# Optimization experiments

Hardware: AMD Instinct MI355X
Metric: run time of the kernel (lower is better)

Reference implementation:

```python
import jax, jax.numpy as jnp
import numpy as np

B, NS, NC = 4096, 1024, 256
GUMBEL_HARD = True


def _linear(x, W, b):
    # torch nn.Linear: y = x @ W.T + b, W is [out, in]
    return x @ W.T + b


def _gumbel_softmax(logits, gnoise, tau, hard):
    y = jax.nn.softmax((logits + gnoise) / tau, axis=-1)
    if hard:
        y_hard = jax.nn.one_hot(jnp.argmax(y, axis=-1), y.shape[-1], dtype=y.dtype)
        y = y_hard + y - jax.lax.stop_gradient(y)  # straight-through
    return y


def setup_inputs() -> dict:
    key = jax.random.key(0)
    ks = jax.random.split(key, 32)
    inp = {
        "ct": jax.random.normal(ks[0], (B, NC), jnp.float32),
        "b1": jax.random.uniform(ks[1], (B, 2), jnp.float32),
        "b2": jax.random.uniform(ks[2], (B, 2), jnp.float32),
        "b3": jax.random.uniform(ks[3], (B, 2), jnp.float32),
        "rnn1": jax.random.normal(ks[4], (B, NS), jnp.float32),
        "rnn2": jax.random.normal(ks[5], (B, NS), jnp.float32),
        "rnn3": jax.random.normal(ks[6], (B, NS), jnp.float32),
        "rnn4": jax.random.normal(ks[7], (B, NS), jnp.float32),
        "gn1": jax.random.gumbel(ks[8], (B, 2), jnp.float32),
        "gn2": jax.random.gumbel(ks[9], (B, 2), jnp.float32),
        "gn3": jax.random.gumbel(ks[10], (B, 2), jnp.float32),
        "theta": 1,
    }
    def lin(k, out_d, in_d):
        return (0.02 * jax.random.normal(k, (out_d, in_d), jnp.float32),
                jnp.zeros((out_d,), jnp.float32))
    shapes = {
        "e_ct": (NS, NC), "rnn1_b0": (NS, 2 * NS), "rnn1_b1": (NS, 2 * NS),
        "b1_rnn1": (2, NS), "rnn2_b0": (NS, 2 * NS), "rnn2_b1": (NS, 2 * NS),
        "b2_rnn2": (2, NS), "rnn3_b0": (NS, 2 * NS), "rnn3_b1": (NS, 2 * NS),
        "b3_rnn3": (2, NS), "rnn4": (NS, 2 * NS), "hg_rnns": (NS, 4 * NS),
        "g_hg": (4, NS), "hctpi_rnns": (NS, 4 * NS), "ctpi_hctpi": (NC, NS),
    }
    for i, (name, (o, ii)) in enumerate(shapes.items()):
        W, bb = lin(ks[11 + i], o, ii)
        inp["W_" + name] = W
        inp["b_" + name] = bb
    return inp


def reference(ct, b1, b2, b3, rnn1, rnn2, rnn3, rnn4, gn1, gn2, gn3, theta,
              W_e_ct, b_e_ct, W_rnn1_b0, b_rnn1_b0, W_rnn1_b1, b_rnn1_b1,
              W_b1_rnn1, b_b1_rnn1, W_rnn2_b0, b_rnn2_b0, W_rnn2_b1, b_rnn2_b1,
              W_b2_rnn2, b_b2_rnn2, W_rnn3_b0, b_rnn3_b0, W_rnn3_b1, b_rnn3_b1,
              W_b3_rnn3, b_b3_rnn3, W_rnn4, b_rnn4, W_hg_rnns, b_hg_rnns,
              W_g_hg, b_g_hg, W_hctpi_rnns, b_hctpi_rnns, W_ctpi_hctpi, b_ctpi_hctpi):
    tau = jnp.float32(theta)
    b1tm1f = b1[:, 0:1]
    ct_e = jax.nn.relu(_linear(ct, W_e_ct, b_e_ct))

    rnn1b1 = jnp.tanh(_linear(jnp.concatenate((rnn2, ct_e), axis=1), W_rnn1_b1, b_rnn1_b1))
    rnn1b0 = jnp.tanh(_linear(jnp.concatenate((rnn1, ct_e), axis=1), W_rnn1_b0, b_rnn1_b0))
    rnn1t = b1tm1f * rnn1b1 + (1.0 - b1tm1f) * rnn1b0
    b1t = _gumbel_softmax(_linear(rnn1t, W_b1_rnn1, b_b1_rnn1), gn1, tau, GUMBEL_HARD)
    b1tf = b1t[:, 0:1]

    b2tm1f = b2[:, 0:1]
    rnn2b1 = jnp.tanh(_linear(jnp.concatenate((rnn3, rnn1t), axis=1), W_rnn2_b1, b_rnn2_b1))
    rnn2b0 = jnp.tanh(_linear(jnp.concatenate((rnn2, rnn1t), axis=1), W_rnn2_b0, b_rnn2_b0))
    rnn2_inner = (1.0 - b2tm1f) * rnn2b0 + b2tm1f * rnn2b1
    rnn2t = (1.0 - b1tf) * rnn2 + b1tf * rnn2_inner
    b2tnew = _gumbel_softmax(_linear(rnn2t, W_b2_rnn2, b_b2_rnn2), gn2, tau, GUMBEL_HARD)
    b2t = b1tf * b2tnew + (1.0 - b1tf) * b2
    b2tf = b2t[:, 0:1]

    b3tm1f = b3[:, 0:1]
    rnn3b1 = jnp.tanh(_linear(jnp.concatenate((rnn4, rnn2t), axis=1), W_rnn3_b1, b_rnn3_b1))
    rnn3b0 = jnp.tanh(_linear(jnp.concatenate((rnn3, rnn2t), axis=1), W_rnn3_b0, b_rnn3_b0))
    rnn3_inner = b3tm1f * rnn3b1 + (1.0 - b3tm1f) * rnn3b0
    rnn3t = (1.0 - b1tf) * rnn3 + b1tf * ((1.0 - b2tf) * rnn3 + b2tf * rnn3_inner)
    b3tnew = _gumbel_softmax(_linear(rnn3t, W_b3_rnn3, b_b3_rnn3), gn3, tau, GUMBEL_HARD)
    b3t = b1tf * (b2tf * b3tnew + (1.0 - b2tf) * b3) + (1.0 - b1tf) * b3
    b3tf = b3t[:, 0:1]

    rnn4_inner = jnp.tanh(_linear(jnp.concatenate((rnn4, rnn3t), axis=1), W_rnn4, b_rnn4))
    rnn4t = (1.0 - b1tf) * rnn4 + b1tf * ((1.0 - b2tf) * rnn4 + b2tf * ((1.0 - b3tf) * rnn4 + b3tf * rnn4_inner))

    hg = jax.nn.relu(_linear(jnp.concatenate((rnn1t, rnn2t, rnn3t, rnn4t), axis=1), W_hg_rnns, b_hg_rnns))
    g = jax.nn.sigmoid(_linear(hg, W_g_hg, b_g_hg))
    gated = jnp.concatenate((g[:, 0:1] * rnn1t, g[:, 1:2] * rnn2t, g[:, 2:3] * rnn3t, g[:, 3:4] * rnn4t), axis=1)
    hctpi = jax.nn.relu(_linear(gated, W_hctpi_rnns, b_hctpi_rnns))
    ctpi = jax.nn.log_softmax(_linear(hctpi, W_ctpi_hctpi, b_ctpi_hctpi), axis=1)
    return (ctpi, b1t, b2t, b3t, rnn1t, rnn2t, rnn3t, rnn4t)
```

## Files before the change

kernel.cpp:

```cpp
#include <hip/hip_runtime.h>
#include <cstdint>
#include <cstddef>

typedef unsigned short u16;
typedef __bf16 bf16x8 __attribute__((ext_vector_type(8)));
typedef float  f32x4  __attribute__((ext_vector_type(4)));
typedef u16    u16x4  __attribute__((ext_vector_type(4)));

__device__ __forceinline__ void splitv(const float4 a, const float4 b, bf16x8& h, bf16x8& l) {
    float x[8] = {a.x, a.y, a.z, a.w, b.x, b.y, b.z, b.w};
#pragma unroll
    for (int i = 0; i < 8; i++) {
        __bf16 hh = (__bf16)x[i];
        h[i] = hh;
        l[i] = (__bf16)(x[i] - (float)hh);
    }
}
__device__ __forceinline__ void hiv(const float4 a, const float4 b, bf16x8& h) {
    float x[8] = {a.x, a.y, a.z, a.w, b.x, b.y, b.z, b.w};
#pragma unroll
    for (int i = 0; i < 8; i++) h[i] = (__bf16)x[i];
}

__device__ __forceinline__ void gl16(const void* g, void* l) {
    __builtin_amdgcn_global_load_lds((__attribute__((address_space(1))) void*)g,
                                     (__attribute__((address_space(3))) void*)l, 16, 0, 0);
}

struct Sec {
    const void* h;
    const u16*  l;
    int lda; int mode;
};
struct GemmArgs {
    Sec A0[4]; Sec A1[4];
    const u16* B0h; const u16* B0l;
    const u16* B1h; const u16* B1l;
    const float* bias0; const float* bias1;
    float* Z0; float* Z1;
    u16* Zh0; u16* Zl0; u16* Zh1; u16* Zl1;
    int bk[4];
    int nsec, ldb, N, spsl, relu, zmode;
};

template <int NP>
__global__ __launch_bounds__(256, 2) void gemm_v6(GemmArgs p) {
    constexpr bool NP3 = (NP == 3);
    __shared__ __align__(16) u16 AhS[2][4096];
    __shared__ __align__(16) u16 BhS[2][4096];
    __shared__ __align__(16) u16 AlS[NP3 ? 2 : 1][NP3 ? 4096 : 8];
    __shared__ __align__(16) u16 BlS[NP3 ? 2 : 1][NP3 ? 4096 : 8];

    const int tid = threadIdx.x;
    const int lin = blockIdx.x;
    const int mt = ((lin & 7) << 2) | ((lin >> 3) & 3);
    const int nt = lin >> 5;
    const int NTh = p.N >> 7;
    const int half = (nt >= NTh) ? 1 : 0;
    const int n0 = (nt - (half ? NTh : 0)) * 128;
    const int m0 = mt * 128;
    const u16* Bwh = half ? p.B1h : p.B0h;
    const u16* Bwl = half ? p.B1l : p.B0l;
    const float* bia = half ? p.bias1 : p.bias0;
    float* Z = half ? p.Z1 : p.Z0;
    u16* Zh = half ? p.Zh1 : p.Zh0;
    u16* Zl = half ? p.Zl1 : p.Zl0;
    const Sec* As = half ? p.A1 : p.A0;

    const int wave = tid >> 6, lane = tid & 63;
    const int quad = lane >> 4, lr = lane & 15;
    const int wm = (wave & 1) * 64, wn = (wave >> 1) * 64;

    f32x4 acc[4][4];
#pragma unroll
    for (int i = 0; i < 4; i++)
#pragma unroll
        for (int j = 0; j < 4; j++) acc[i][j] = (f32x4){0.f, 0.f, 0.f, 0.f};

    const int arow = tid >> 2;
    const int aslot = tid & 3;
    const int csw = aslot ^ ((arow ^ (arow >> 2)) & 3);
    const int wr_i0 = arow * 32 + csw * 8;
    const int ldsw = wave * 1024;
    const int qx8 = ((quad ^ ((lr ^ (lr >> 2)) & 3)) & 3) * 8;

    const int sps = 1 << p.spsl;
    const int total = p.nsec << p.spsl;

    float4 v0a{}, v0b{}, v1a{}, v1b{};

    auto regload = [&](const Sec& sec, int t) {
        const float* a0 = (const float*)sec.h + (size_t)(m0 + arow) * sec.lda + t * 32 + aslot * 8;
        v0a = ((const float4*)a0)[0]; v0b = ((const float4*)a0)[1];
        const float* a1 = a0 + (size_t)64 * sec.lda;
        v1a = ((const float4*)a1)[0]; v1b = ((const float4*)a1)[1];
    };
    auto writeA0 = [&](int buf) {
        if constexpr (NP3) {
            bf16x8 h, l;
            splitv(v0a, v0b, h, l);
            *(bf16x8*)&AhS[buf][wr_i0] = h;        *(bf16x8*)&AlS[buf][wr_i0] = l;
            splitv(v1a, v1b, h, l);
            *(bf16x8*)&AhS[buf][2048 + wr_i0] = h; *(bf16x8*)&AlS[buf][2048 + wr_i0] = l;
        } else {
            bf16x8 h;
            hiv(v0a, v0b, h); *(bf16x8*)&AhS[buf][wr_i0] = h;
            hiv(v1a, v1b, h); *(bf16x8*)&AhS[buf][2048 + wr_i0] = h;
        }
    };
    auto stageA1 = [&](int buf, const Sec& sec, int t) {
        const u16* gh = (const u16*)sec.h;
        const size_t o0 = (size_t)(m0 + arow) * sec.lda + t * 32 + csw * 8;
        const size_t o1 = o0 + (size_t)64 * sec.lda;
        gl16(gh + o0, (char*)&AhS[buf][0] + ldsw);
        gl16(gh + o1, (char*)&AhS[buf][0] + 4096 + ldsw);
        if constexpr (NP3) {
            gl16(sec.l + o0, (char*)&AlS[buf][0] + ldsw);
            gl16(sec.l + o1, (char*)&AlS[buf][0] + 4096 + ldsw);
        }
    };
    auto stageB = [&](int buf, int s, int t) {
        const size_t o0 = (size_t)(n0 + arow) * p.ldb + p.bk[s] + t * 32 + csw * 8;
        const size_t o1 = o0 + (size_t)64 * p.ldb;
        gl16(Bwh + o0, (char*)&BhS[buf][0] + ldsw);
        gl16(Bwh + o1, (char*)&BhS[buf][0] + 4096 + ldsw);
        if constexpr (NP3) {
            gl16(Bwl + o0, (char*)&BlS[buf][0] + ldsw);
            gl16(Bwl + o1, (char*)&BlS[buf][0] + 4096 + ldsw);
        }
    };

    stageB(0, 0, 0);
    {
        const Sec s0 = As[0];
        if (s0.mode == 0) { regload(s0, 0); writeA0(0); }
        else stageA1(0, s0, 0);
    }
    if (total > 1) {
        const Sec s1 = As[1 >> p.spsl];
        if (s1.mode == 0) regload(s1, 1 & (sps - 1));
    }
    __syncthreads();

    for (int tt = 0; tt < total; ++tt) {
        const int cur = tt & 1, nxt = cur ^ 1;
        if (tt + 1 < total) {
            const int u = tt + 1, s = u >> p.spsl, t = u & (sps - 1);
            stageB(nxt, s, t);
            const Sec sec = As[s];
            if (sec.mode == 0) writeA0(nxt);
            else stageA1(nxt, sec, t);
            if (tt + 2 < total) {
                const int s2 = (tt + 2) >> p.spsl;
                const Sec sec2 = As[s2];
                if (sec2.mode == 0) regload(sec2, (tt + 2) & (sps - 1));
            }
        }
        bf16x8 ah[4], bh[4];
#pragma unroll
        for (int i = 0; i < 4; i++)
            ah[i] = *reinterpret_cast<const bf16x8*>(&AhS[cur][(wm + i * 16 + lr) * 32 + qx8]);
#pragma unroll
        for (int j = 0; j < 4; j++)
            bh[j] = *reinterpret_cast<const bf16x8*>(&BhS[cur][(wn + j * 16 + lr) * 32 + qx8]);
#pragma unroll
        for (int i = 0; i < 4; i++)
#pragma unroll
            for (int j = 0; j < 4; j++)
                acc[i][j] = __builtin_amdgcn_mfma_f32_16x16x32_bf16(ah[i], bh[j], acc[i][j], 0, 0, 0);
        if constexpr (NP3) {
            bf16x8 al[4], bl[4];
#pragma unroll
            for (int i = 0; i < 4; i++)
                al[i] = *reinterpret_cast<const bf16x8*>(&AlS[cur][(wm + i * 16 + lr) * 32 + qx8]);
#pragma unroll
            for (int j = 0; j < 4; j++)
                bl[j] = *reinterpret_cast<const bf16x8*>(&BlS[cur][(wn + j * 16 + lr) * 32 + qx8]);
#pragma unroll
            for (int i = 0; i < 4; i++)
#pragma unroll
                for (int j = 0; j < 4; j++) {
                    acc[i][j] = __builtin_amdgcn_mfma_f32_16x16x32_bf16(ah[i], bl[j], acc[i][j], 0, 0, 0);
                    acc[i][j] = __builtin_amdgcn_mfma_f32_16x16x32_bf16(al[i], bh[j], acc[i][j], 0, 0, 0);
                }
        }
        __syncthreads();
    }

#pragma unroll
    for (int j = 0; j < 4; j++) {
        const int n = n0 + wn + j * 16 + lr;
        const float bj = bia[n];
#pragma unroll
        for (int i = 0; i < 4; i++)
#pragma unroll
            for (int r = 0; r < 4; r++) {
                const int m = m0 + wm + i * 16 + quad * 4 + r;
                float v = acc[i][j][r] + bj;
                if (p.relu) v = fmaxf(v, 0.f);
                const size_t zi = (size_t)m * p.N + n;
                if (p.zmode == 0) {
                    Z[zi] = v;
                } else {
                    __bf16 hb = (__bf16)v;
                    Zh[zi] = __builtin_bit_cast(u16, hb);
                    if (p.zmode == 2)
                        Zl[zi] = __builtin_bit_cast(u16, (__bf16)(v - (float)hb));
                }
            }
    }
}

__global__ __launch_bounds__(256) void conv_split(const float* x0, u16* h0, u16* l0, int n0v,
                                                  const float* x1, u16* h1, u16* l1, int n1v) {
    int i = blockIdx.x * 256 + threadIdx.x;
    const float* x; u16* h; u16* l;
    if (i < n0v) { x = x0; h = h0; l = l0; }
    else { i -= n0v; if (i >= n1v) return; x = x1; h = h1; l = l1; }
    const float4 a = ((const float4*)x)[2 * i], b = ((const float4*)x)[2 * i + 1];
    bf16x8 hh, ll;
    if (l) { splitv(a, b, hh, ll); ((bf16x8*)h)[i] = hh; ((bf16x8*)l)[i] = ll; }
    else   { hiv(a, b, hh);        ((bf16x8*)h)[i] = hh; }
}

__device__ __forceinline__ void store_hl4(const float4 o, u16* hp, u16* lp, int base) {
    float xs[4] = {o.x, o.y, o.z, o.w};
    u16x4 hv, lv;
#pragma unroll
    for (int k = 0; k < 4; k++) {
        __bf16 hb = (__bf16)xs[k];
        hv[k] = __builtin_bit_cast(u16, hb);
        if (lp) lv[k] = __builtin_bit_cast(u16, (__bf16)(xs[k] - (float)hb));
    }
    *(u16x4*)(hp + base) = hv;
    if (lp) *(u16x4*)(lp + base) = lv;
}

__global__ __launch_bounds__(256) void combine1(const float* Z0, const float* Z1, const float* b1in,
                                                float* outr, u16* hO, u16* lO) {
    const int base = (blockIdx.x * 256 + threadIdx.x) * 4;
    const int m = base >> 10;
    const float bf = b1in[2 * m];
    const float4 z0 = *(const float4*)(Z0 + base), z1 = *(const float4*)(Z1 + base);
    float4 o;
    o.x = bf * tanhf(z1.x) + (1.f - bf) * tanhf(z0.x);
    o.y = bf * tanhf(z1.y) + (1.f - bf) * tanhf(z0.y);
    o.z = bf * tanhf(z1.z) + (1.f - bf) * tanhf(z0.z);
    o.w = bf * tanhf(z1.w) + (1.f - bf) * tanhf(z0.w);
    *(float4*)(outr + base) = o;
    store_hl4(o, hO, lO, base);
}
__global__ __launch_bounds__(256) void combine2(const float* Z0, const float* Z1, const float* b2in,
                                                const float* rnn2in, const float* F1, float* outr,
                                                u16* hO, u16* lO) {
    const int base = (blockIdx.x * 256 + threadIdx.x) * 4;
    const int m = base >> 10;
    const float b2f = b2in[2 * m], f1 = F1[m];
    const float4 z0 = *(const float4*)(Z0 + base), z1 = *(const float4*)(Z1 + base);
    const float4 r2 = *(const float4*)(rnn2in + base);
    float4 o;
    o.x = (1.f - f1) * r2.x + f1 * ((1.f - b2f) * tanhf(z0.x) + b2f * tanhf(z1.x));
    o.y = (1.f - f1) * r2.y + f1 * ((1.f - b2f) * tanhf(z0.y) + b2f * tanhf(z1.y));
    o.z = (1.f - f1) * r2.z + f1 * ((1.f - b2f) * tanhf(z0.z) + b2f * tanhf(z1.z));
    o.w = (1.f - f1) * r2.w + f1 * ((1.f - b2f) * tanhf(z0.w) + b2f * tanhf(z1.w));
    *(float4*)(outr + base) = o;
    store_hl4(o, hO, lO, base);
}
__global__ __launch_bounds__(256) void combine3(const float* Z0, const float* Z1, const float* b3in,
                                                const float* rnn3in, const float* F1, const float* F2,
                                                float* outr, u16* hO) {
    const int base = (blockIdx.x * 256 + threadIdx.x) * 4;
    const int m = base >> 10;
    const float b3f = b3in[2 * m], f1 = F1[m], f2 = F2[m];
    const float4 z0 = *(const float4*)(Z0 + base), z1 = *(const float4*)(Z1 + base);
    const float4 r3 = *(const float4*)(rnn3in + base);
    float4 o;
    o.x = (1.f - f1) * r3.x + f1 * ((1.f - f2) * r3.x + f2 * (b3f * tanhf(z1.x) + (1.f - b3f) * tanhf(z0.x)));
    o.y = (1.f - f1) * r3.y + f1 * ((1.f - f2) * r3.y + f2 * (b3f * tanhf(z1.y) + (1.f - b3f) * tanhf(z0.y)));
    o.z = (1.f - f1) * r3.z + f1 * ((1.f - f2) * r3.z + f2 * (b3f * tanhf(z1.z) + (1.f - b3f) * tanhf(z0.z)));
    o.w = (1.f - f1) * r3.w + f1 * ((1.f - f2) * r3.w + f2 * (b3f * tanhf(z1.w) + (1.f - b3f) * tanhf(z0.w)));
    *(float4*)(outr + base) = o;
    store_hl4(o, hO, nullptr, base);
}
__global__ __launch_bounds__(256) void combine4(const float* Z0, const float* rnn4in, const float* F1,
                                                const float* F2, const float* F3, float* outr, u16* hO) {
    const int base = (blockIdx.x * 256 + threadIdx.x) * 4;
    const int m = base >> 10;
    const float f1 = F1[m], f2 = F2[m], f3 = F3[m];
    const float4 z0 = *(const float4*)(Z0 + base);
    const float4 r4 = *(const float4*)(rnn4in + base);
    float4 o;
    o.x = (1.f - f1) * r4.x + f1 * ((1.f - f2) * r4.x + f2 * ((1.f - f3) * r4.x + f3 * tanhf(z0.x)));
    o.y = (1.f - f1) * r4.y + f1 * ((1.f - f2) * r4.y + f2 * ((1.f - f3) * r4.y + f3 * tanhf(z0.y)));
    o.z = (1.f - f1) * r4.z + f1 * ((1.f - f2) * r4.z + f2 * ((1.f - f3) * r4.z + f3 * tanhf(z0.z)));
    o.w = (1.f - f1) * r4.w + f1 * ((1.f - f2) * r4.w + f2 * ((1.f - f3) * r4.w + f3 * tanhf(z0.w)));
    *(float4*)(outr + base) = o;
    store_hl4(o, hO, nullptr, base);
}

__global__ __launch_bounds__(256) void gemv_decide(const float* x, const float* W2, const float* bias2,
                                                   const float* gn, const float* bprev,
                                                   const float* Fp1, const float* Fp2,
                                                   float* bout, float* fout, int stage) {
    const int wave = threadIdx.x >> 6, lane = threadIdx.x & 63;
    const int m = blockIdx.x * 4 + wave;
    const float* row = x + (size_t)m * 1024;
    float s0 = 0.f, s1 = 0.f;
#pragma unroll 4
    for (int i = 0; i < 16; i++) {
        const int k = lane + 64 * i;
        const float v = row[k];
        s0 += v * W2[k];
        s1 += v * W2[1024 + k];
    }
    for (int off = 32; off > 0; off >>= 1) { s0 += __shfl_xor(s0, off); s1 += __shfl_xor(s1, off); }
    if (lane == 0) {
        const float l0 = s0 + bias2[0] + gn[2 * m];
        const float l1 = s1 + bias2[1] + gn[2 * m + 1];
        const float nf = (l0 >= l1) ? 1.f : 0.f;
        float v0, v1;
        if (stage == 1) {
            v0 = nf; v1 = 1.f - nf;
        } else if (stage == 2) {
            const float f1 = Fp1[m];
            const float p0 = bprev[2 * m], p1 = bprev[2 * m + 1];
            v0 = f1 * nf + (1.f - f1) * p0;
            v1 = f1 * (1.f - nf) + (1.f - f1) * p1;
        } else {
            const float f1 = Fp1[m], f2 = Fp2[m];
            const float p0 = bprev[2 * m], p1 = bprev[2 * m + 1];
            const float i0 = f2 * nf + (1.f - f2) * p0;
            const float i1 = f2 * (1.f - nf) + (1.f - f2) * p1;
            v0 = f1 * i0 + (1.f - f1) * p0;
            v1 = f1 * i1 + (1.f - f1) * p1;
        }
        fout[m] = v0;
        bout[2 * m] = v0; bout[2 * m + 1] = v1;
    }
}

__global__ __launch_bounds__(256) void gemv_g4(const float* hg, const float* Wg, const float* bg, float* G) {
    const int wave = threadIdx.x >> 6, lane = threadIdx.x & 63;
    const int m = blockIdx.x * 4 + wave;
    const float* row = hg + (size_t)m * 1024;
    float s[4] = {0.f, 0.f, 0.f, 0.f};
#pragma unroll 4
    for (int i = 0; i < 16; i++) {
        const int k = lane + 64 * i;
        const float v = row[k];
#pragma unroll
        for (int j = 0; j < 4; j++) s[j] += v * Wg[j * 1024 + k];
    }
    for (int off = 32; off > 0; off >>= 1)
#pragma unroll
        for (int j = 0; j < 4; j++) s[j] += __shfl_xor(s[j], off);
    if (lane == 0) {
#pragma unroll
        for (int j = 0; j < 4; j++) G[m * 4 + j] = 1.f / (1.f + expf(-(s[j] + bg[j])));
    }
}

__global__ __launch_bounds__(256) void gated_k(const float* rnnF, const float* G, u16* gatedh) {
    const int base = (blockIdx.x * 256 + threadIdx.x) * 4;
    const int m = base >> 12, rem = base & 4095;
    const int j = rem >> 10, k = rem & 1023;
    const float g = G[m * 4 + j];
    const float4 r = *(const float4*)(rnnF + (size_t)j * 4194304 + (size_t)m * 1024 + k);
    u16x4 hv;
    hv[0] = __builtin_bit_cast(u16, (__bf16)(g * r.x));
    hv[1] = __builtin_bit_cast(u16, (__bf16)(g * r.y));
    hv[2] = __builtin_bit_cast(u16, (__bf16)(g * r.z));
    hv[3] = __builtin_bit_cast(u16, (__bf16)(g * r.w));
    *(u16x4*)(gatedh + base) = hv;
}

__global__ __launch_bounds__(256) void logsoftmax_k(const float* Z, float* out) {
    const int wave = threadIdx.x >> 6, lane = threadIdx.x & 63;
    const int row = blockIdx.x * 4 + wave;
    const size_t base = (size_t)row * 256;
    float x[4];
#pragma unroll
    for (int i = 0; i < 4; i++) x[i] = Z[base + lane + 64 * i];
    float mx = fmaxf(fmaxf(x[0], x[1]), fmaxf(x[2], x[3]));
    for (int off = 32; off > 0; off >>= 1) mx = fmaxf(mx, __shfl_xor(mx, off));
    float s = 0.f;
#pragma unroll
    for (int i = 0; i < 4; i++) s += expf(x[i] - mx);
    for (int off = 32; off > 0; off >>= 1) s += __shfl_xor(s, off);
    const float lse = mx + logf(s);
#pragma unroll
    for (int i = 0; i < 4; i++) out[base + lane + 64 * i] = x[i] - lse;
}

static const size_t OUT_B1 = 1048576, OUT_B2 = 1056768, OUT_B3 = 1064960;
static const size_t OUT_R1 = 1073152, OUT_R2 = 5267456, OUT_R3 = 9461760, OUT_R4 = 13656064;

static inline Sec S0(const float* f, int lda) { Sec s; s.h = f; s.l = nullptr; s.lda = lda; s.mode = 0; return s; }
static inline Sec S1(const u16* h, const u16* l, int lda) { Sec s; s.h = h; s.l = l; s.lda = lda; s.mode = 1; return s; }

extern "C" void kernel_launch(void* const* d_in, const int* in_sizes, int n_in,
                              void* d_out, int out_size, void* d_ws, size_t ws_size,
                              hipStream_t stream) {
    (void)in_sizes; (void)n_in; (void)out_size; (void)ws_size;
    const float* ct   = (const float*)d_in[0];
    const float* b1   = (const float*)d_in[1];
    const float* b2   = (const float*)d_in[2];
    const float* b3   = (const float*)d_in[3];
    const float* rnn1 = (const float*)d_in[4];
    const float* rnn2 = (const float*)d_in[5];
    const float* rnn3 = (const float*)d_in[6];
    const float* rnn4 = (const float*)d_in[7];
    const float* gn1  = (const float*)d_in[8];
    const float* gn2  = (const float*)d_in[9];
    const float* gn3  = (const float*)d_in[10];
    const float* W_e    = (const float*)d_in[12]; const float* be    = (const float*)d_in[13];
    const float* W_r1b0 = (const float*)d_in[14]; const float* br1b0 = (const float*)d_in[15];
    const float* W_r1b1 = (const float*)d_in[16]; const float* br1b1 = (const float*)d_in[17];
    const float* W_b1   = (const float*)d_in[18]; const float* bb1   = (const float*)d_in[19];
    const float* W_r2b0 = (const float*)d_in[20]; const float* br2b0 = (const float*)d_in[21];
    const float* W_r2b1 = (const float*)d_in[22]; const float* br2b1 = (const float*)d_in[23];
    const float* W_b2   = (const float*)d_in[24]; const float* bb2   = (const float*)d_in[25];
    const float* W_r3b0 = (const float*)d_in[26]; const float* br3b0 = (const float*)d_in[27];
    const float* W_r3b1 = (const float*)d_in[28]; const float* br3b1 = (const float*)d_in[29];
    const float* W_b3   = (const float*)d_in[30]; const float* bb3   = (const float*)d_in[31];
    const float* W_r4   = (const float*)d_in[32]; const float* br4   = (const float*)d_in[33];
    const float* W_hg   = (const float*)d_in[34]; const float* bhg   = (const float*)d_in[35];
    const float* W_g    = (const float*)d_in[36]; const float* bg    = (const float*)d_in[37];
    const float* W_hct  = (const float*)d_in[38]; const float* bhct  = (const float*)d_in[39];
    const float* W_ct   = (const float*)d_in[40]; const float* bct   = (const float*)d_in[41];

    float* out = (float*)d_out;
    char* w = (char*)d_ws;
    const size_t MB = 1024 * 1024;
    float* Z0    = (float*)(w);
    float* Z1    = (float*)(w + 16 * MB);
    u16* WS      = (u16*)(w + 32 * MB);
    u16* CTEFh   = (u16*)(w + 48 * MB);
    u16* CTEFl   = (u16*)(w + 56 * MB);
    u16* R1h     = (u16*)(w + 64 * MB);
    u16* R1l     = (u16*)(w + 72 * MB);
    u16* R2h     = (u16*)(w + 48 * MB);
    u16* R2l     = (u16*)(w + 56 * MB);
    u16* R3h     = (u16*)(w + 72 * MB);
    u16* R4h     = (u16*)(w + 56 * MB);
    float* HGF   = (float*)(w);
    u16* GATEDh  = (u16*)(w);
    u16* HCTFh   = (u16*)(w + 48 * MB);
    float* ZC    = (float*)(w);
    float* F1 = out; float* F2 = F1 + 4096; float* F3 = F1 + 8192; float* G4 = F1 + 12288;
    float* R1 = out + OUT_R1; float* R2 = out + OUT_R2;
    float* R3 = out + OUT_R3; float* R4 = out + OUT_R4;

    const int NWe = 32768, NWr = 262144, NWg = 524288, NWct = 32768;
    auto conv = [&](const float* x0, u16* h0, u16* l0, int n0v,
                    const float* x1, u16* h1, u16* l1, int n1v) {
        const int tot = n0v + n1v;
        conv_split<<<dim3((tot + 255) / 256), 256, 0, stream>>>(x0, h0, l0, n0v, x1, h1, l1, n1v);
    };
    auto launch = [&](const GemmArgs& p, int NT, int npass) {
        if (npass == 3) gemm_v6<3><<<dim3(NT * 32), 256, 0, stream>>>(p);
        else            gemm_v6<1><<<dim3(NT * 32), 256, 0, stream>>>(p);
    };
    const dim3 EW(4096), GV(1024);

    conv(W_e, WS, WS + 262144, NWe, nullptr, nullptr, nullptr, 0);
    {
        GemmArgs p{};
        p.A0[0] = S0(ct, 256); p.A1[0] = p.A0[0];
        p.B0h = WS; p.B0l = WS + 262144; p.B1h = p.B0h; p.B1l = p.B0l;
        p.bias0 = be; p.bias1 = be;
        p.Zh0 = CTEFh; p.Zl0 = CTEFl; p.Zh1 = CTEFh; p.Zl1 = CTEFl;
        p.bk[0] = 0; p.nsec = 1; p.ldb = 256; p.N = 1024; p.spsl = 3;
        p.relu = 1; p.zmode = 2;
        launch(p, 8, 3);
    }
    conv(W_r1b0, WS, WS + 2097152, NWr, W_r1b1, WS + 4194304, WS + 6291456, NWr);
    {
        GemmArgs p{};
        p.A0[0] = S0(rnn1, 1024); p.A0[1] = S1(CTEFh, CTEFl, 1024);
        p.A1[0] = S0(rnn2, 1024); p.A1[1] = p.A0[1];
        p.B0h = WS; p.B0l = WS + 2097152; p.B1h = WS + 4194304; p.B1l = WS + 6291456;
        p.bias0 = br1b0; p.bias1 = br1b1;
        p.Z0 = Z0; p.Z1 = Z1;
        p.bk[0] = 0; p.bk[1] = 1024; p.nsec = 2; p.ldb = 2048; p.N = 1024; p.spsl = 5;
        p.relu = 0; p.zmode = 0;
        launch(p, 16, 3);
    }
    combine1<<<EW, 256, 0, stream>>>(Z0, Z1, b1, R1, R1h, R1l);
    gemv_decide<<<GV, 256, 0, stream>>>(R1, W_b1, bb1, gn1, b1, F1, F1, out + OUT_B1, F1, 1);
    conv(W_r2b0, WS, WS + 2097152, NWr, W_r2b1, WS + 4194304, WS + 6291456, NWr);
    {
        GemmArgs p{};
        p.A0[0] = S0(rnn2, 1024); p.A0[1] = S1(R1h, R1l, 1024);
        p.A1[0] = S0(rnn3, 1024); p.A1[1] = p.A0[1];
        p.B0h = WS; p.B0l = WS + 2097152; p.B1h = WS + 4194304; p.B1l = WS + 6291456;
        p.bias0 = br2b0; p.bias1 = br2b1;
        p.Z0 = Z0; p.Z1 = Z1;
        p.bk[0] = 0; p.bk[1] = 1024; p.nsec = 2; p.ldb = 2048; p.N = 1024; p.spsl = 5;
        p.relu = 0; p.zmode = 0;
        launch(p, 16, 3);
    }
    combine2<<<EW, 256, 0, stream>>>(Z0, Z1, b2, rnn2, F1, R2, R2h, R2l);
    gemv_decide<<<GV, 256, 0, stream>>>(R2, W_b2, bb2, gn2, b2, F1, F1, out + OUT_B2, F2, 2);
    conv(W_r3b0, WS, WS + 2097152, NWr, W_r3b1, WS + 4194304, WS + 6291456, NWr);
    {
        GemmArgs p{};
        p.A0[0] = S0(rnn3, 1024); p.A0[1] = S1(R2h, R2l, 1024);
        p.A1[0] = S0(rnn4, 1024); p.A1[1] = p.A0[1];
        p.B0h = WS; p.B0l = WS + 2097152; p.B1h = WS + 4194304; p.B1l = WS + 6291456;
        p.bias0 = br3b0; p.bias1 = br3b1;
        p.Z0 = Z0; p.Z1 = Z1;
        p.bk[0] = 0; p.bk[1] = 1024; p.nsec = 2; p.ldb = 2048; p.N = 1024; p.spsl = 5;
        p.relu = 0; p.zmode = 0;
        launch(p, 16, 3);
    }
    combine3<<<EW, 256, 0, stream>>>(Z0, Z1, b3, rnn3, F1, F2, R3, R3h);
    gemv_decide<<<GV, 256, 0, stream>>>(R3, W_b3, bb3, gn3, b3, F1, F2, out + OUT_B3, F3, 3);
    conv(W_r4, WS, nullptr, NWr, nullptr, nullptr, nullptr, 0);
    {
        GemmArgs p{};
        p.A0[0] = S0(rnn4, 1024); p.A0[1] = S1(R3h, nullptr, 1024);
        p.A1[0] = p.A0[0]; p.A1[1] = p.A0[1];
        p.B0h = WS; p.B0l = nullptr; p.B1h = WS; p.B1l = nullptr;
        p.bias0 = br4; p.bias1 = br4;
        p.Z0 = Z0; p.Z1 = Z0;
        p.bk[0] = 0; p.bk[1] = 1024; p.nsec = 2; p.ldb = 2048; p.N = 1024; p.spsl = 5;
        p.relu = 0; p.zmode = 0;
        launch(p, 8, 1);
    }
    combine4<<<EW, 256, 0, stream>>>(Z0, rnn4, F1, F2, F3, R4, R4h);
    conv(W_hg, WS, nullptr, NWg, nullptr, nullptr, nullptr, 0);
    {
        GemmArgs p{};
        p.A0[0] = S1(R1h, nullptr, 1024); p.A0[1] = S1(R2h, nullptr, 1024);
        p.A0[2] = S1(R3h, nullptr, 1024); p.A0[3] = S1(R4h, nullptr, 1024);
        p.A1[0] = p.A0[0]; p.A1[1] = p.A0[1]; p.A1[2] = p.A0[2]; p.A1[3] = p.A0[3];
        p.B0h = WS; p.B1h = WS;
        p.bias0 = bhg; p.bias1 = bhg;
        p.Z0 = HGF; p.Z1 = HGF;
        p.bk[0] = 0; p.bk[1] = 1024; p.bk[2] = 2048; p.bk[3] = 3072;
        p.nsec = 4; p.ldb = 4096; p.N = 1024; p.spsl = 5;
        p.relu = 1; p.zmode = 0;
        launch(p, 8, 1);
    }
    gemv_g4<<<GV, 256, 0, stream>>>(HGF, W_g, bg, G4);
    gated_k<<<dim3(16384), 256, 0, stream>>>(R1, G4, GATEDh);
    conv(W_hct, WS, nullptr, NWg, nullptr, nullptr, nullptr, 0);
    {
        GemmArgs p{};
        p.A0[0] = S1(GATEDh, nullptr, 4096); p.A1[0] = p.A0[0];
        p.B0h = WS; p.B1h = WS;
        p.bias0 = bhct; p.bias1 = bhct;
        p.Zh0 = HCTFh; p.Zh1 = HCTFh;
        p.bk[0] = 0; p.nsec = 1; p.ldb = 4096; p.N = 1024; p.spsl = 7;
        p.relu = 1; p.zmode = 1;
        launch(p, 8, 1);
    }
    conv(W_ct, WS, nullptr, NWct, nullptr, nullptr, nullptr, 0);
    {
        GemmArgs p{};
        p.A0[0] = S1(HCTFh, nullptr, 1024); p.A1[0] = p.A0[0];
        p.B0h = WS; p.B1h = WS;
        p.bias0 = bct; p.bias1 = bct;
        p.Z0 = ZC; p.Z1 = ZC;
        p.bk[0] = 0; p.nsec = 1; p.ldb = 1024; p.N = 256; p.spsl = 5;
        p.relu = 0; p.zmode = 0;
        launch(p, 2, 1);
    }
    logsoftmax_k<<<GV, 256, 0, stream>>>(ZC, out);
}
```

Before: 940.5 us.

## Replace GEMM syncthreads with explicit vmcnt waits, raw barriers and MFMA priority

The double-buffered GEMM main loop drops the full __syncthreads, which drains all outstanding memory operations. It now issues the next stage's global-to-LDS loads first, then waits with s_waitcnt vmcnt(N) only until the current buffer's loads have landed, and synchronises with raw s_barrier calls. This lets next-tile prefetches stay in flight across the barrier. s_setprio is raised around the MFMA block to favour math issue. The final logits GEMM launch grid is doubled, so the second half recomputes and rewrites the same tiles (B1, bias1 and Z1 alias the first half). That adds redundant work, and the hand-counted vmcnt values are fragile if the load count per stage changes.

```diff
diff --git a/kernel.cpp b/kernel.cpp
--- a/kernel.cpp
+++ b/kernel.cpp
@@ -44,7 +44,7 @@
 };
 
 template <int NP>
-__global__ __launch_bounds__(256, 2) void gemm_v6(GemmArgs p) {
+__global__ __launch_bounds__(256, 2) void gemm_v7(GemmArgs p) {
     constexpr bool NP3 = (NP == 3);
     __shared__ __align__(16) u16 AhS[2][4096];
     __shared__ __align__(16) u16 BhS[2][4096];
@@ -140,22 +140,39 @@
         const Sec s1 = As[1 >> p.spsl];
         if (s1.mode == 0) regload(s1, 1 & (sps - 1));
     }
-    __syncthreads();
 
     for (int tt = 0; tt < total; ++tt) {
         const int cur = tt & 1, nxt = cur ^ 1;
         if (tt + 1 < total) {
             const int u = tt + 1, s = u >> p.spsl, t = u & (sps - 1);
-            stageB(nxt, s, t);
             const Sec sec = As[s];
-            if (sec.mode == 0) writeA0(nxt);
-            else stageA1(nxt, sec, t);
-            if (tt + 2 < total) {
-                const int s2 = (tt + 2) >> p.spsl;
-                const Sec sec2 = As[s2];
-                if (sec2.mode == 0) regload(sec2, (tt + 2) & (sps - 1));
+            if (sec.mode == 0) {
+                stageB(nxt, s, t);
+                if constexpr (NP3) asm volatile("s_waitcnt vmcnt(4)" ::: "memory");
+                else               asm volatile("s_waitcnt vmcnt(2)" ::: "memory");
+                __builtin_amdgcn_sched_barrier(0);
+                writeA0(nxt);
+                if (tt + 2 < total) {
+                    const Sec sec2 = As[(tt + 2) >> p.spsl];
+                    if (sec2.mode == 0) regload(sec2, (tt + 2) & (sps - 1));
+                }
+            } else {
+                stageB(nxt, s, t);
+                stageA1(nxt, sec, t);
+                if constexpr (NP3) asm volatile("s_waitcnt vmcnt(8)" ::: "memory");
+                else               asm volatile("s_waitcnt vmcnt(4)" ::: "memory");
+                __builtin_amdgcn_sched_barrier(0);
+                if (tt + 2 < total) {
+                    const Sec sec2 = As[(tt + 2) >> p.spsl];
+                    if (sec2.mode == 0) regload(sec2, (tt + 2) & (sps - 1));
+                }
             }
+        } else {
+            asm volatile("s_waitcnt vmcnt(0)" ::: "memory");
+            __builtin_amdgcn_sched_barrier(0);
         }
+        asm volatile("s_waitcnt lgkmcnt(0)" ::: "memory");
+        __builtin_amdgcn_s_barrier();
         bf16x8 ah[4], bh[4];
 #pragma unroll
         for (int i = 0; i < 4; i++)
@@ -163,6 +180,7 @@
 #pragma unroll
         for (int j = 0; j < 4; j++)
             bh[j] = *reinterpret_cast<const bf16x8*>(&BhS[cur][(wn + j * 16 + lr) * 32 + qx8]);
+        __builtin_amdgcn_s_setprio(1);
 #pragma unroll
         for (int i = 0; i < 4; i++)
 #pragma unroll
@@ -184,7 +202,9 @@
                     acc[i][j] = __builtin_amdgcn_mfma_f32_16x16x32_bf16(al[i], bh[j], acc[i][j], 0, 0, 0);
                 }
         }
-        __syncthreads();
+        __builtin_amdgcn_s_setprio(0);
+        __builtin_amdgcn_sched_barrier(0);
+        __builtin_amdgcn_s_barrier();
     }
 
 #pragma unroll
@@ -458,8 +478,8 @@
         conv_split<<<dim3((tot + 255) / 256), 256, 0, stream>>>(x0, h0, l0, n0v, x1, h1, l1, n1v);
     };
     auto launch = [&](const GemmArgs& p, int NT, int npass) {
-        if (npass == 3) gemm_v6<3><<<dim3(NT * 32), 256, 0, stream>>>(p);
-        else            gemm_v6<1><<<dim3(NT * 32), 256, 0, stream>>>(p);
+        if (npass == 3) gemm_v7<3><<<dim3(NT * 32), 256, 0, stream>>>(p);
+        else            gemm_v7<1><<<dim3(NT * 32), 256, 0, stream>>>(p);
     };
     const dim3 EW(4096), GV(1024);
 
@@ -565,7 +585,7 @@
         p.Z0 = ZC; p.Z1 = ZC;
         p.bk[0] = 0; p.nsec = 1; p.ldb = 1024; p.N = 256; p.spsl = 5;
         p.relu = 0; p.zmode = 0;
-        launch(p, 2, 1);
+        launch(p, 4, 1);
     }
     logsoftmax_k<<<GV, 256, 0, stream>>>(ZC, out);
 }
```

After: 1.037 ms. 10.3% more time.

## Use 128x64 tiles with two K-steps per barrier for single-pass GEMMs

Applied to the files above, without the earlier changes.

For the single-pass bf16 GEMM path, the N tile shrinks from 128 to 64 and the grid doubles, so more blocks run across the CUs. Each pipeline stage now stages two 32-wide K slices before a barrier, which halves the number of __syncthreads per K sweep. The cost is less reuse of each A tile, since A is loaded twice as often across N, plus more shared memory and registers per block. The 3-pass path keeps the old 128x128 tiling.

```diff
diff --git a/kernel.cpp b/kernel.cpp
--- a/kernel.cpp
+++ b/kernel.cpp
@@ -44,10 +44,14 @@
 };
 
 template <int NP>
-__global__ __launch_bounds__(256, 2) void gemm_v6(GemmArgs p) {
+__global__ __launch_bounds__(256, 2) void gemm_v8(GemmArgs p) {
     constexpr bool NP3 = (NP == 3);
-    __shared__ __align__(16) u16 AhS[2][4096];
-    __shared__ __align__(16) u16 BhS[2][4096];
+    constexpr int G  = NP3 ? 1 : 2;
+    constexpr int BN = NP3 ? 128 : 64;
+    constexpr int NJ = NP3 ? 4 : 2;
+    constexpr int BROWS = BN;
+    __shared__ __align__(16) u16 AhS[2][G][4096];
+    __shared__ __align__(16) u16 BhS[2][G][BROWS * 32];
     __shared__ __align__(16) u16 AlS[NP3 ? 2 : 1][NP3 ? 4096 : 8];
     __shared__ __align__(16) u16 BlS[NP3 ? 2 : 1][NP3 ? 4096 : 8];
 
@@ -55,9 +59,9 @@
     const int lin = blockIdx.x;
     const int mt = ((lin & 7) << 2) | ((lin >> 3) & 3);
     const int nt = lin >> 5;
-    const int NTh = p.N >> 7;
+    const int NTh = p.N / BN;
     const int half = (nt >= NTh) ? 1 : 0;
-    const int n0 = (nt - (half ? NTh : 0)) * 128;
+    const int n0 = (nt - (half ? NTh : 0)) * BN;
     const int m0 = mt * 128;
     const u16* Bwh = half ? p.B1h : p.B0h;
     const u16* Bwl = half ? p.B1l : p.B0l;
@@ -69,13 +73,14 @@
 
     const int wave = tid >> 6, lane = tid & 63;
     const int quad = lane >> 4, lr = lane & 15;
-    const int wm = (wave & 1) * 64, wn = (wave >> 1) * 64;
-
-    f32x4 acc[4][4];
+    const int wm = (wave & 1) * 64;
+    const int wn = (wave >> 1) * (NP3 ? 64 : 32);
+
+    f32x4 acc[4][NJ];
 #pragma unroll
     for (int i = 0; i < 4; i++)
 #pragma unroll
-        for (int j = 0; j < 4; j++) acc[i][j] = (f32x4){0.f, 0.f, 0.f, 0.f};
+        for (int j = 0; j < NJ; j++) acc[i][j] = (f32x4){0.f, 0.f, 0.f, 0.f};
 
     const int arow = tid >> 2;
     const int aslot = tid & 3;
@@ -86,109 +91,128 @@
 
     const int sps = 1 << p.spsl;
     const int total = p.nsec << p.spsl;
-
-    float4 v0a{}, v0b{}, v1a{}, v1b{};
-
-    auto regload = [&](const Sec& sec, int t) {
+    const int ng = total / G;
+
+    float4 v[G][4];
+#pragma unroll
+    for (int k = 0; k < G; k++)
+#pragma unroll
+        for (int q = 0; q < 4; q++) v[k][q] = (float4){0.f, 0.f, 0.f, 0.f};
+
+    auto regload = [&](int k, const Sec& sec, int t) {
         const float* a0 = (const float*)sec.h + (size_t)(m0 + arow) * sec.lda + t * 32 + aslot * 8;
-        v0a = ((const float4*)a0)[0]; v0b = ((const float4*)a0)[1];
+        v[k][0] = ((const float4*)a0)[0]; v[k][1] = ((const float4*)a0)[1];
         const float* a1 = a0 + (size_t)64 * sec.lda;
-        v1a = ((const float4*)a1)[0]; v1b = ((const float4*)a1)[1];
+        v[k][2] = ((const float4*)a1)[0]; v[k][3] = ((const float4*)a1)[1];
     };
-    auto writeA0 = [&](int buf) {
+    auto writeA0 = [&](int buf, int k) {
         if constexpr (NP3) {
             bf16x8 h, l;
-            splitv(v0a, v0b, h, l);
-            *(bf16x8*)&AhS[buf][wr_i0] = h;        *(bf16x8*)&AlS[buf][wr_i0] = l;
-            splitv(v1a, v1b, h, l);
-            *(bf16x8*)&AhS[buf][2048 + wr_i0] = h; *(bf16x8*)&AlS[buf][2048 + wr_i0] = l;
+            splitv(v[k][0], v[k][1], h, l);
+            *(bf16x8*)&AhS[buf][0][wr_i0] = h;        *(bf16x8*)&AlS[buf][wr_i0] = l;
+            splitv(v[k][2], v[k][3], h, l);
+            *(bf16x8*)&AhS[buf][0][2048 + wr_i0] = h; *(bf16x8*)&AlS[buf][2048 + wr_i0] = l;
         } else {
             bf16x8 h;
-            hiv(v0a, v0b, h); *(bf16x8*)&AhS[buf][wr_i0] = h;
-            hiv(v1a, v1b, h); *(bf16x8*)&AhS[buf][2048 + wr_i0] = h;
+            hiv(v[k][0], v[k][1], h); *(bf16x8*)&AhS[buf][k][wr_i0] = h;
+            hiv(v[k][2], v[k][3], h); *(bf16x8*)&AhS[buf][k][2048 + wr_i0] = h;
         }
     };
-    auto stageA1 = [&](int buf, const Sec& sec, int t) {
+    auto stageA1 = [&](int buf, int k, const Sec& sec, int t) {
         const u16* gh = (const u16*)sec.h;
         const size_t o0 = (size_t)(m0 + arow) * sec.lda + t * 32 + csw * 8;
         const size_t o1 = o0 + (size_t)64 * sec.lda;
-        gl16(gh + o0, (char*)&AhS[buf][0] + ldsw);
-        gl16(gh + o1, (char*)&AhS[buf][0] + 4096 + ldsw);
+        gl16(gh + o0, (char*)&AhS[buf][k][0] + ldsw);
+        gl16(gh + o1, (char*)&AhS[buf][k][0] + 4096 + ldsw);
         if constexpr (NP3) {
             gl16(sec.l + o0, (char*)&AlS[buf][0] + ldsw);
             gl16(sec.l + o1, (char*)&AlS[buf][0] + 4096 + ldsw);
         }
     };
-    auto stageB = [&](int buf, int s, int t) {
+    auto stageB = [&](int buf, int k, int s, int t) {
         const size_t o0 = (size_t)(n0 + arow) * p.ldb + p.bk[s] + t * 32 + csw * 8;
-        const size_t o1 = o0 + (size_t)64 * p.ldb;
-        gl16(Bwh + o0, (char*)&BhS[buf][0] + ldsw);
-        gl16(Bwh + o1, (char*)&BhS[buf][0] + 4096 + ldsw);
+        gl16(Bwh + o0, (char*)&BhS[buf][k][0] + ldsw);
         if constexpr (NP3) {
+            const size_t o1 = o0 + (size_t)64 * p.ldb;
+            gl16(Bwh + o1, (char*)&BhS[buf][k][0] + 4096 + ldsw);
             gl16(Bwl + o0, (char*)&BlS[buf][0] + ldsw);
             gl16(Bwl + o1, (char*)&BlS[buf][0] + 4096 + ldsw);
         }
     };
 
-    stageB(0, 0, 0);
-    {
+#pragma unroll
+    for (int k = 0; k < G; k++) {
+        stageB(0, k, 0, k);
         const Sec s0 = As[0];
-        if (s0.mode == 0) { regload(s0, 0); writeA0(0); }
-        else stageA1(0, s0, 0);
-    }
-    if (total > 1) {
-        const Sec s1 = As[1 >> p.spsl];
-        if (s1.mode == 0) regload(s1, 1 & (sps - 1));
+        if (s0.mode == 0) { regload(k, s0, k); writeA0(0, k); }
+        else stageA1(0, k, s0, k);
+    }
+#pragma unroll
+    for (int k = 0; k < G; k++) {
+        const int u = G + k;
+        if (u < total) {
+            const Sec s1 = As[u >> p.spsl];
+            if (s1.mode == 0) regload(k, s1, u & (sps - 1));
+        }
     }
     __syncthreads();
 
-    for (int tt = 0; tt < total; ++tt) {
-        const int cur = tt & 1, nxt = cur ^ 1;
-        if (tt + 1 < total) {
-            const int u = tt + 1, s = u >> p.spsl, t = u & (sps - 1);
-            stageB(nxt, s, t);
-            const Sec sec = As[s];
-            if (sec.mode == 0) writeA0(nxt);
-            else stageA1(nxt, sec, t);
-            if (tt + 2 < total) {
-                const int s2 = (tt + 2) >> p.spsl;
-                const Sec sec2 = As[s2];
-                if (sec2.mode == 0) regload(sec2, (tt + 2) & (sps - 1));
+    for (int gg = 0; gg < ng; ++gg) {
+        const int cur = gg & 1, nxt = cur ^ 1;
+        if (gg + 1 < ng) {
+#pragma unroll
+            for (int k = 0; k < G; k++) {
+                const int u = (gg + 1) * G + k, s = u >> p.spsl, t = u & (sps - 1);
+                stageB(nxt, k, s, t);
+                const Sec sec = As[s];
+                if (sec.mode == 0) writeA0(nxt, k);
+                else stageA1(nxt, k, sec, t);
             }
-        }
-        bf16x8 ah[4], bh[4];
-#pragma unroll
-        for (int i = 0; i < 4; i++)
-            ah[i] = *reinterpret_cast<const bf16x8*>(&AhS[cur][(wm + i * 16 + lr) * 32 + qx8]);
-#pragma unroll
-        for (int j = 0; j < 4; j++)
-            bh[j] = *reinterpret_cast<const bf16x8*>(&BhS[cur][(wn + j * 16 + lr) * 32 + qx8]);
-#pragma unroll
-        for (int i = 0; i < 4; i++)
-#pragma unroll
-            for (int j = 0; j < 4; j++)
-                acc[i][j] = __builtin_amdgcn_mfma_f32_16x16x32_bf16(ah[i], bh[j], acc[i][j], 0, 0, 0);
-        if constexpr (NP3) {
-            bf16x8 al[4], bl[4];
+#pragma unroll
+            for (int k = 0; k < G; k++) {
+                const int u2 = (gg + 2) * G + k;
+                if (u2 < total) {
+                    const Sec sec2 = As[u2 >> p.spsl];
+                    if (sec2.mode == 0) regload(k, sec2, u2 & (sps - 1));
+                }
+            }
+        }
+#pragma unroll
+        for (int k = 0; k < G; k++) {
+            bf16x8 ah[4], bh[NJ];
 #pragma unroll
             for (int i = 0; i < 4; i++)
-                al[i] = *reinterpret_cast<const bf16x8*>(&AlS[cur][(wm + i * 16 + lr) * 32 + qx8]);
-#pragma unroll
-            for (int j = 0; j < 4; j++)
-                bl[j] = *reinterpret_cast<const bf16x8*>(&BlS[cur][(wn + j * 16 + lr) * 32 + qx8]);
+                ah[i] = *reinterpret_cast<const bf16x8*>(&AhS[cur][k][(wm + i * 16 + lr) * 32 + qx8]);
+#pragma unroll
+            for (int j = 0; j < NJ; j++)
+                bh[j] = *reinterpret_cast<const bf16x8*>(&BhS[cur][k][(wn + j * 16 + lr) * 32 + qx8]);
 #pragma unroll
             for (int i = 0; i < 4; i++)
 #pragma unroll
-                for (int j = 0; j < 4; j++) {
-                    acc[i][j] = __builtin_amdgcn_mfma_f32_16x16x32_bf16(ah[i], bl[j], acc[i][j], 0, 0, 0);
-                    acc[i][j] = __builtin_amdgcn_mfma_f32_16x16x32_bf16(al[i], bh[j], acc[i][j], 0, 0, 0);
-                }
+                for (int j = 0; j < NJ; j++)
+                    acc[i][j] = __builtin_amdgcn_mfma_f32_16x16x32_bf16(ah[i], bh[j], acc[i][j], 0, 0, 0);
+            if constexpr (NP3) {
+                bf16x8 al[4], bl[NJ];
+#pragma unroll
+                for (int i = 0; i < 4; i++)
+                    al[i] = *reinterpret_cast<const bf16x8*>(&AlS[cur][(wm + i * 16 + lr) * 32 + qx8]);
+#pragma unroll
+                for (int j = 0; j < NJ; j++)
+                    bl[j] = *reinterpret_cast<const bf16x8*>(&BlS[cur][(wn + j * 16 + lr) * 32 + qx8]);
+#pragma unroll
+                for (int i = 0; i < 4; i++)
+#pragma unroll
+                    for (int j = 0; j < NJ; j++) {
+                        acc[i][j] = __builtin_amdgcn_mfma_f32_16x16x32_bf16(ah[i], bl[j], acc[i][j], 0, 0, 0);
+                        acc[i][j] = __builtin_amdgcn_mfma_f32_16x16x32_bf16(al[i], bh[j], acc[i][j], 0, 0, 0);
+                    }
+            }
         }
         __syncthreads();
     }
 
 #pragma unroll
-    for (int j = 0; j < 4; j++) {
+    for (int j = 0; j < NJ; j++) {
         const int n = n0 + wn + j * 16 + lr;
         const float bj = bia[n];
 #pragma unroll
@@ -196,16 +220,16 @@
 #pragma unroll
             for (int r = 0; r < 4; r++) {
                 const int m = m0 + wm + i * 16 + quad * 4 + r;
-                float v = acc[i][j][r] + bj;
-                if (p.relu) v = fmaxf(v, 0.f);
+                float v2 = acc[i][j][r] + bj;
+                if (p.relu) v2 = fmaxf(v2, 0.f);
                 const size_t zi = (size_t)m * p.N + n;
                 if (p.zmode == 0) {
-                    Z[zi] = v;
+                    Z[zi] = v2;
                 } else {
-                    __bf16 hb = (__bf16)v;
+                    __bf16 hb = (__bf16)v2;
                     Zh[zi] = __builtin_bit_cast(u16, hb);
                     if (p.zmode == 2)
-                        Zl[zi] = __builtin_bit_cast(u16, (__bf16)(v - (float)hb));
+                        Zl[zi] = __builtin_bit_cast(u16, (__bf16)(v2 - (float)hb));
                 }
             }
     }
@@ -458,8 +482,8 @@
         conv_split<<<dim3((tot + 255) / 256), 256, 0, stream>>>(x0, h0, l0, n0v, x1, h1, l1, n1v);
     };
     auto launch = [&](const GemmArgs& p, int NT, int npass) {
-        if (npass == 3) gemm_v6<3><<<dim3(NT * 32), 256, 0, stream>>>(p);
-        else            gemm_v6<1><<<dim3(NT * 32), 256, 0, stream>>>(p);
+        if (npass == 3) gemm_v8<3><<<dim3(NT * 32), 256, 0, stream>>>(p);
+        else            gemm_v8<1><<<dim3(NT * 32), 256, 0, stream>>>(p);
     };
     const dim3 EW(4096), GV(1024);
 
@@ -526,7 +550,7 @@
         p.Z0 = Z0; p.Z1 = Z0;
         p.bk[0] = 0; p.bk[1] = 1024; p.nsec = 2; p.ldb = 2048; p.N = 1024; p.spsl = 5;
         p.relu = 0; p.zmode = 0;
-        launch(p, 8, 1);
+        launch(p, 16, 1);
     }
     combine4<<<EW, 256, 0, stream>>>(Z0, rnn4, F1, F2, F3, R4, R4h);
     conv(W_hg, WS, nullptr, NWg, nullptr, nullptr, nullptr, 0);
@@ -541,7 +565,7 @@
         p.bk[0] = 0; p.bk[1] = 1024; p.bk[2] = 2048; p.bk[3] = 3072;
         p.nsec = 4; p.ldb = 4096; p.N = 1024; p.spsl = 5;
         p.relu = 1; p.zmode = 0;
-        launch(p, 8, 1);
+        launch(p, 16, 1);
     }
     gemv_g4<<<GV, 256, 0, stream>>>(HGF, W_g, bg, G4);
     gated_k<<<dim3(16384), 256, 0, stream>>>(R1, G4, GATEDh);
@@ -554,7 +578,7 @@
         p.Zh0 = HCTFh; p.Zh1 = HCTFh;
         p.bk[0] = 0; p.nsec = 1; p.ldb = 4096; p.N = 1024; p.spsl = 7;
         p.relu = 1; p.zmode = 1;
-        launch(p, 8, 1);
+        launch(p, 16, 1);
     }
     conv(W_ct, WS, nullptr, NWct, nullptr, nullptr, nullptr, 0);
     {
@@ -565,7 +589,7 @@
         p.Z0 = ZC; p.Z1 = ZC;
         p.bk[0] = 0; p.nsec = 1; p.ldb = 1024; p.N = 256; p.spsl = 5;
         p.relu = 0; p.zmode = 0;
-        launch(p, 2, 1);
+        launch(p, 4, 1);
     }
     logsoftmax_k<<<GV, 256, 0, stream>>>(ZC, out);
 }
```

After: 882.8 us. 1.07x faster.
